# Kernel optimization log

Measured on AMD Instinct MI355X. Metric: run time of the kernel, lower is better.

Reference implementation:

```python
import jax, jax.numpy as jnp
import numpy as np

SEQ, BATCH, EMBED = 1024, 2, 768
E = 16            # num_experts = m * N = 2 * 8
FFN_H = 1536      # expert_dim = ceil(3072 / 2)
K_SHARED = 1
K_ROUTE = 3       # (m * top_k) - k_shared = 4 - 1
LN_EPS = 1e-5
NEG_INF = -1e9


def setup_inputs() -> dict:
    key = jax.random.key(0)
    ks = jax.random.split(key, 4)
    x = jax.random.normal(ks[0], (SEQ, BATCH, EMBED), dtype=jnp.float32)
    gate_w = jax.random.normal(ks[1], (EMBED, E), dtype=jnp.float32) * 0.02
    gate_b = jnp.zeros((E,), jnp.float32)
    fc1_w = jax.random.normal(ks[2], (E, EMBED, FFN_H), dtype=jnp.float32) * 0.02
    fc1_b = jnp.zeros((E, FFN_H), jnp.float32)
    ln_w = jnp.ones((E, FFN_H), jnp.float32)
    ln_b = jnp.zeros((E, FFN_H), jnp.float32)
    fc2_w = jax.random.normal(ks[3], (E, FFN_H, EMBED), dtype=jnp.float32) * 0.02
    fc2_b = jnp.zeros((E, EMBED), jnp.float32)
    return {"x": x, "gate_w": gate_w, "gate_b": gate_b,
            "fc1_w": fc1_w, "fc1_b": fc1_b, "ln_w": ln_w, "ln_b": ln_b,
            "fc2_w": fc2_w, "fc2_b": fc2_b}


def reference(x, gate_w, gate_b, fc1_w, fc1_b, ln_w, ln_b, fc2_w, fc2_b):
    S, B, D = x.shape
    T = S * B
    xf = x.reshape(T, D)

    # --- gating: mask shared-expert logits, softmax, top-k over routed probs ---
    scores = xf @ gate_w + gate_b                      # [T, E]
    scores = scores.at[:, :K_SHARED].set(NEG_INF)
    probs = jax.nn.softmax(scores, axis=-1)
    topv, topi = jax.lax.top_k(probs, K_ROUTE)         # [T, K_ROUTE]

    # combine weights: gate prob for selected routed experts, 1.0 for shared experts
    combine = jnp.zeros((T, E), xf.dtype)
    combine = combine.at[jnp.arange(T)[:, None], topi].add(topv)
    combine = combine.at[:, :K_SHARED].add(1.0)        # shared expert(s), weight 1

    # --- per-expert FFN (dense over experts; combine zeros out unselected) ---
    h = jnp.einsum('td,edh->eth', xf, fc1_w) + fc1_b[:, None, :]   # [E, T, H]
    h = jax.nn.gelu(h, approximate=False)              # torch nn.GELU = exact erf
    mu = h.mean(-1, keepdims=True)
    var = h.var(-1, keepdims=True)
    h = (h - mu) * jax.lax.rsqrt(var + LN_EPS) * ln_w[:, None, :] + ln_b[:, None, :]
    y = jnp.einsum('eth,ehd->etd', h, fc2_w) + fc2_b[:, None, :]   # [E, T, D]

    # --- scatter-add combine (gate-weighted sum over experts) ---
    out = jnp.einsum('te,etd->td', combine, y)
    return out.reshape(S, B, D)
```

## Files before the change

kernel.cpp:

```cpp
#include <hip/hip_runtime.h>
#include <cmath>

#define T_TOK 2048
#define D_EMB 768
#define H_FFN 1536
#define NE    16
#define NPAIR (T_TOK * 4)

typedef __attribute__((ext_vector_type(8))) short          short8;
typedef __attribute__((ext_vector_type(8))) unsigned short ushort8;
typedef __attribute__((ext_vector_type(4))) unsigned short ushort4v;
typedef __attribute__((ext_vector_type(4))) float          floatx4;

__device__ __forceinline__ float bf2f(unsigned short u) {
  union { unsigned int i; float f; } v; v.i = ((unsigned int)u) << 16; return v.f;
}
__device__ __forceinline__ unsigned short f2bf(float f) {
  union { float f; unsigned int i; } v; v.f = f;
  unsigned int r = v.i + 0x7fffu + ((v.i >> 16) & 1u);
  return (unsigned short)(r >> 16);
}

__global__ __launch_bounds__(64) void sniff_kernel(
    const unsigned int* __restrict__ x, int* __restrict__ flag)
{
  int lane = threadIdx.x;
  int c = 0;
  for (int i = 0; i < 8; i++) {
    unsigned int w = x[i * 64 + lane];
    unsigned int e = (w >> 7) & 0xFFu;
    c += (e >= 100u && e <= 140u) ? 1 : 0;
  }
  for (int off = 32; off > 0; off >>= 1) c += __shfl_down(c, off);
  if (lane == 0) *flag = (c > 300) ? 1 : 0;
}

__global__ __launch_bounds__(256) void conv_kernel(
    const float* __restrict__ x, const float* __restrict__ fc1b,
    const float* __restrict__ lnw, const float* __restrict__ lnb,
    const float* __restrict__ fc2b,
    unsigned short* __restrict__ dx, unsigned short* __restrict__ dfc1b,
    unsigned short* __restrict__ dlnw, unsigned short* __restrict__ dlnb,
    unsigned short* __restrict__ dfc2b, const int* __restrict__ flag)
{
  if (*flag) return;
  int g = blockIdx.x * 256 + threadIdx.x;
#pragma unroll
  for (int i = 0; i < 3; i++) dx[g + i * 524288] = f2bf(x[g + i * 524288]);
  if (g < 24576) { dfc1b[g] = f2bf(fc1b[g]); dlnw[g] = f2bf(lnw[g]); dlnb[g] = f2bf(lnb[g]); }
  if (g < 12288) dfc2b[g] = f2bf(fc2b[g]);
}

template<int R, int C>
__global__ __launch_bounds__(256) void transpose_kernel(
    const unsigned short* __restrict__ srcB, const float* __restrict__ srcF,
    const int* __restrict__ flag, unsigned short* __restrict__ dst)
{
  __shared__ __align__(16) unsigned short tile[64][72];
  constexpr int RT = R / 64, CT = C / 64;
  int bx  = blockIdx.x;
  int e   = bx / (RT * CT);
  int rem = bx % (RT * CT);
  int rt  = rem / CT, ct = rem % CT;
  int tid = threadIdx.x;
  int r   = tid >> 2;
  int c   = (tid & 3) * 16;
  int xr  = (r & 7) * 8;
  size_t sbase = ((size_t)e * R + rt * 64 + r) * C + ct * 64 + c;
  if (*flag) {
    ushort8 v0 = *(const ushort8*)(srcB + sbase);
    ushort8 v1 = *(const ushort8*)(srcB + sbase + 8);
    *(ushort8*)&tile[r][(c) ^ xr]     = v0;
    *(ushort8*)&tile[r][(c + 8) ^ xr] = v1;
  } else {
    unsigned short tmp[16];
#pragma unroll
    for (int q = 0; q < 4; q++) {
      floatx4 f = *(const floatx4*)(srcF + sbase + q * 4);
#pragma unroll
      for (int j = 0; j < 4; j++) tmp[q * 4 + j] = f2bf(f[j]);
    }
    *(ushort8*)&tile[r][(c) ^ xr]     = *(ushort8*)&tmp[0];
    *(ushort8*)&tile[r][(c + 8) ^ xr] = *(ushort8*)&tmp[8];
  }
  __syncthreads();
  int n  = tid >> 2;
  int k  = (tid & 3) * 16;
  unsigned short outv[16];
#pragma unroll
  for (int j = 0; j < 16; j++) {
    int kr = k + j;
    outv[j] = tile[kr][n ^ ((kr & 7) * 8)];
  }
  size_t dbase = ((size_t)e * C + ct * 64 + n) * R + rt * 64 + k;
  *(ushort8*)(dst + dbase)     = *(ushort8*)&outv[0];
  *(ushort8*)(dst + dbase + 8) = *(ushort8*)&outv[8];
}

__global__ __launch_bounds__(64) void gate_kernel(
    const unsigned short* __restrict__ x16, const float* __restrict__ x32,
    const unsigned short* __restrict__ gw16, const float* __restrict__ gw32,
    const unsigned short* __restrict__ gb16, const float* __restrict__ gb32,
    const int* __restrict__ flag,
    int* __restrict__ psel, float* __restrict__ pw)
{
  int t = blockIdx.x;
  int lane = threadIdx.x;
  int isbf = *flag;
  float acc[NE];
#pragma unroll
  for (int e = 0; e < NE; e++) acc[e] = 0.f;
  if (isbf) {
#pragma unroll
    for (int i = 0; i < D_EMB / 64; i++) {
      int d = i * 64 + lane;
      float xv = bf2f(x16[(size_t)t * D_EMB + d]);
      ushort8 g0 = *(const ushort8*)(gw16 + d * NE);
      ushort8 g1 = *(const ushort8*)(gw16 + d * NE + 8);
#pragma unroll
      for (int e = 0; e < 8; e++) acc[e]     += xv * bf2f(g0[e]);
#pragma unroll
      for (int e = 0; e < 8; e++) acc[8 + e] += xv * bf2f(g1[e]);
    }
  } else {
#pragma unroll
    for (int i = 0; i < D_EMB / 64; i++) {
      int d = i * 64 + lane;
      float xv = x32[(size_t)t * D_EMB + d];
#pragma unroll
      for (int q = 0; q < 4; q++) {
        floatx4 g = *(const floatx4*)(gw32 + d * NE + q * 4);
#pragma unroll
        for (int j = 0; j < 4; j++) acc[q * 4 + j] += xv * g[j];
      }
    }
  }
  __shared__ __align__(16) float sacc[64][NE + 1];
#pragma unroll
  for (int e = 0; e < NE; e++) sacc[lane][e] = acc[e];
  __syncthreads();
  int e = lane & 15, q = lane >> 4;
  float s = 0.f;
#pragma unroll
  for (int i = 0; i < 16; i++) s += sacc[q * 16 + i][e];
  s += __shfl_xor(s, 16);
  s += __shfl_xor(s, 32);
  float sv = s + (isbf ? bf2f(gb16[e]) : gb32[e]);
  if (e == 0) sv = -1e9f;
  float m = sv;
#pragma unroll
  for (int off = 8; off > 0; off >>= 1) m = fmaxf(m, __shfl_xor(m, off));
  float pe = expf(sv - m);
  float den = pe;
#pragma unroll
  for (int off = 8; off > 0; off >>= 1) den += __shfl_xor(den, off);
  float pr = pe / den;
  float val = (e == 0) ? -1.f : pr;
  int sel0, sel1, sel2; float sw0, sw1, sw2;
#pragma unroll
  for (int k = 0; k < 3; k++) {
    float bv = val; int bi = e;
#pragma unroll
    for (int off = 8; off > 0; off >>= 1) {
      float ov = __shfl_xor(bv, off);
      int   oi = __shfl_xor(bi, off);
      if (ov > bv || (ov == bv && oi < bi)) { bv = ov; bi = oi; }
    }
    if (k == 0) { sel0 = bi; sw0 = bv; }
    else if (k == 1) { sel1 = bi; sw1 = bv; }
    else { sel2 = bi; sw2 = bv; }
    if (e == bi) val = -1.f;
  }
  if (lane == 0) {
    psel[t * 4] = 0;    pw[t * 4] = 1.0f;
    psel[t * 4 + 1] = sel0; pw[t * 4 + 1] = sw0;
    psel[t * 4 + 2] = sel1; pw[t * 4 + 2] = sw1;
    psel[t * 4 + 3] = sel2; pw[t * 4 + 3] = sw2;
  }
}

__global__ __launch_bounds__(256) void bucket_kernel(
    const int* __restrict__ psel, int* __restrict__ cnt, int* __restrict__ plist)
{
  int e = blockIdx.x;
  int tid = threadIdx.x;
  int wave = tid >> 6, lane = tid & 63;
  __shared__ int wsum[4];
  __shared__ int base;
  if (tid == 0) base = 0;
  __syncthreads();
  for (int c0 = 0; c0 < NPAIR; c0 += 256) {
    bool mt = (psel[c0 + tid] == e);
    unsigned long long mask = __ballot(mt);
    int wcount = __popcll(mask);
    if (lane == 0) wsum[wave] = wcount;
    __syncthreads();
    int wpre = 0;
#pragma unroll
    for (int w = 0; w < 4; w++) if (w < wave) wpre += wsum[w];
    int total = wsum[0] + wsum[1] + wsum[2] + wsum[3];
    if (mt) {
      int off = __popcll(mask & ((1ULL << lane) - 1ULL));
      plist[e * T_TOK + base + wpre + off] = c0 + tid;
    }
    __syncthreads();
    if (tid == 0) base += total;
    __syncthreads();
  }
  if (tid == 0) cnt[e] = base;
}

template<int KDIM, int NDIM, bool GELU, bool HASBIAS, bool AROWDIV4, bool OUTF32>
__global__ __launch_bounds__(256) void moe_gemm(
    const unsigned short* __restrict__ AO, const unsigned short* __restrict__ AC,
    const unsigned short* __restrict__ BT,
    const unsigned short* __restrict__ biasO, const unsigned short* __restrict__ biasC,
    const int* __restrict__ flag,
    const int* __restrict__ cnt, const int* __restrict__ plist,
    unsigned short* __restrict__ outB, float* __restrict__ outF)
{
  const int NSP = NDIM / 128;
  int bx  = blockIdx.x;
  int e   = bx / (32 * NSP);
  int rem = bx % (32 * NSP);
  int mt  = rem / NSP;
  int ns  = rem % NSP;
  int count = cnt[e];
  if (mt * 64 >= count) return;
  const unsigned short* Abase   = (*flag) ? AO : AC;
  const unsigned short* biasAll = (*flag) ? biasO : biasC;

  __shared__ __align__(16) unsigned short sA[64][72];
  __shared__ __align__(16) unsigned short sB[128][72];
  __shared__ int sp[64];

  int tid = threadIdx.x;
  if (tid < 64) {
    int rg  = mt * 64 + tid;
    int idx = rg < count ? rg : count - 1;
    sp[tid] = plist[e * T_TOK + idx];
  }
  __syncthreads();

  int arow = tid >> 3;
  int ac8  = (tid & 7) * 8;
  int pr0 = sp[arow], pr1 = sp[arow + 32];
  const unsigned short* Aptr0 = Abase + (size_t)(AROWDIV4 ? (pr0 >> 2) : pr0) * KDIM + ac8;
  const unsigned short* Aptr1 = Abase + (size_t)(AROWDIV4 ? (pr1 >> 2) : pr1) * KDIM + ac8;
  int n0 = ns * 128;
  const unsigned short* Bptr =
      BT + ((size_t)e * NDIM + n0 + arow) * KDIM + ac8;

  int lane = tid & 63;
  int wave = tid >> 6;
  int wm   = (wave >> 1) * 32;
  int wn   = (wave & 1) * 64;
  int m16  = lane & 15;
  int quad = lane >> 4;

  floatx4 acc[2][4];
#pragma unroll
  for (int i = 0; i < 2; i++)
#pragma unroll
    for (int j = 0; j < 4; j++) acc[i][j] = (floatx4){0.f, 0.f, 0.f, 0.f};

  ushort8 pa0 = *(const ushort8*)(Aptr0);
  ushort8 pa1 = *(const ushort8*)(Aptr1);
  ushort8 pb0 = *(const ushort8*)(Bptr);
  ushort8 pb1 = *(const ushort8*)(Bptr + (size_t)32 * KDIM);
  ushort8 pb2 = *(const ushort8*)(Bptr + (size_t)64 * KDIM);
  ushort8 pb3 = *(const ushort8*)(Bptr + (size_t)96 * KDIM);

  for (int k0 = 0; k0 < KDIM; k0 += 64) {
    __syncthreads();
    *(ushort8*)&sA[arow][ac8]       = pa0;
    *(ushort8*)&sA[arow + 32][ac8]  = pa1;
    *(ushort8*)&sB[arow][ac8]       = pb0;
    *(ushort8*)&sB[arow + 32][ac8]  = pb1;
    *(ushort8*)&sB[arow + 64][ac8]  = pb2;
    *(ushort8*)&sB[arow + 96][ac8]  = pb3;
    __syncthreads();
    if (k0 + 64 < KDIM) {
      pa0 = *(const ushort8*)(Aptr0 + k0 + 64);
      pa1 = *(const ushort8*)(Aptr1 + k0 + 64);
      pb0 = *(const ushort8*)(Bptr + k0 + 64);
      pb1 = *(const ushort8*)(Bptr + k0 + 64 + (size_t)32 * KDIM);
      pb2 = *(const ushort8*)(Bptr + k0 + 64 + (size_t)64 * KDIM);
      pb3 = *(const ushort8*)(Bptr + k0 + 64 + (size_t)96 * KDIM);
    }
#pragma unroll
    for (int ks = 0; ks < 2; ks++) {
      short8 af0 = *(const short8*)&sA[wm + m16][ks * 32 + quad * 8];
      short8 af1 = *(const short8*)&sA[wm + 16 + m16][ks * 32 + quad * 8];
#pragma unroll
      for (int nt = 0; nt < 4; nt++) {
        short8 bfg = *(const short8*)&sB[wn + nt * 16 + m16][ks * 32 + quad * 8];
        acc[0][nt] = __builtin_amdgcn_mfma_f32_16x16x32_bf16(af0, bfg, acc[0][nt], 0, 0, 0);
        acc[1][nt] = __builtin_amdgcn_mfma_f32_16x16x32_bf16(af1, bfg, acc[1][nt], 0, 0, 0);
      }
    }
  }
#pragma unroll
  for (int sub = 0; sub < 2; sub++) {
#pragma unroll
    for (int nt = 0; nt < 4; nt++) {
#pragma unroll
      for (int r = 0; r < 4; r++) {
        int row_local = wm + sub * 16 + quad * 4 + r;
        int rg = mt * 64 + row_local;
        if (rg < count) {
          int col = n0 + wn + nt * 16 + m16;
          float v = acc[sub][nt][r];
          if (HASBIAS) v += bf2f(biasAll[e * NDIM + col]);
          if (GELU)    v = 0.5f * v * (1.f + erff(v * 0.70710678118654752f));
          int p = sp[row_local];
          if (OUTF32) outF[(size_t)p * NDIM + col] = v;
          else        outB[(size_t)p * NDIM + col] = f2bf(v);
        }
      }
    }
  }
}

__global__ __launch_bounds__(256) void ln_kernel(
    unsigned short* __restrict__ Hbuf,
    const unsigned short* __restrict__ lnwO, const unsigned short* __restrict__ lnwC,
    const unsigned short* __restrict__ lnbO, const unsigned short* __restrict__ lnbC,
    const int* __restrict__ psel, const float* __restrict__ pw,
    const int* __restrict__ flag)
{
  int p = blockIdx.x;
  int tid = threadIdx.x;
  int e = psel[p];
  int isbf = *flag;
  const unsigned short* lnw = isbf ? lnwO : lnwC;
  const unsigned short* lnb = isbf ? lnbO : lnbC;
  unsigned short* hr = Hbuf + (size_t)p * H_FFN;
  bool act = tid < 192;
  float v[8];
  float s = 0.f, sq = 0.f;
  if (act) {
    ushort8 hv = *(const ushort8*)(hr + tid * 8);
#pragma unroll
    for (int j = 0; j < 8; j++) { v[j] = bf2f(hv[j]); s += v[j]; sq += v[j] * v[j]; }
  }
#pragma unroll
  for (int off = 32; off > 0; off >>= 1) {
    s  += __shfl_down(s, off);
    sq += __shfl_down(sq, off);
  }
  __shared__ float red[8];
  int wave = tid >> 6, lane = tid & 63;
  if (lane == 0) { red[wave * 2] = s; red[wave * 2 + 1] = sq; }
  __syncthreads();
  __shared__ float mv[2];
  if (tid == 0) {
    float S = 0.f, Q = 0.f;
    for (int w = 0; w < 4; w++) { S += red[w * 2]; Q += red[w * 2 + 1]; }
    float mu  = S * (1.f / H_FFN);
    float var = Q * (1.f / H_FFN) - mu * mu;
    mv[0] = mu; mv[1] = rsqrtf(var + 1e-5f);
  }
  __syncthreads();
  if (act) {
    float mu = mv[0], rstd = mv[1];
    float w = pw[p];
    ushort8 lw = *(const ushort8*)(lnw + e * H_FFN + tid * 8);
    ushort8 lb = *(const ushort8*)(lnb + e * H_FFN + tid * 8);
    ushort8 o;
#pragma unroll
    for (int j = 0; j < 8; j++)
      o[j] = f2bf(((v[j] - mu) * rstd * bf2f(lw[j]) + bf2f(lb[j])) * w);
    *(ushort8*)(hr + tid * 8) = o;
  }
}

__global__ __launch_bounds__(256) void combine_kernel(
    const float* __restrict__ Y,
    const unsigned short* __restrict__ b2O, const unsigned short* __restrict__ b2C,
    const int* __restrict__ psel, const float* __restrict__ pw,
    unsigned short* __restrict__ out16, float* __restrict__ out32,
    const int* __restrict__ flag)
{
  int t = blockIdx.x;
  int tid = threadIdx.x;
  if (tid >= 192) return;
  int isbf = *flag;
  const unsigned short* b2 = isbf ? b2O : b2C;
  int e1 = psel[t * 4 + 1], e2 = psel[t * 4 + 2], e3 = psel[t * 4 + 3];
  float w1 = pw[t * 4 + 1], w2 = pw[t * 4 + 2], w3 = pw[t * 4 + 3];
  int d = tid * 4;
  const float* Yb = Y + (size_t)t * 4 * D_EMB + d;
  floatx4 y0 = *(const floatx4*)(Yb);
  floatx4 y1 = *(const floatx4*)(Yb + D_EMB);
  floatx4 y2 = *(const floatx4*)(Yb + 2 * D_EMB);
  floatx4 y3 = *(const floatx4*)(Yb + 3 * D_EMB);
  ushort4v b0 = *(const ushort4v*)(b2 + d);
  ushort4v bb1 = *(const ushort4v*)(b2 + e1 * D_EMB + d);
  ushort4v bb2 = *(const ushort4v*)(b2 + e2 * D_EMB + d);
  ushort4v bb3 = *(const ushort4v*)(b2 + e3 * D_EMB + d);
  if (isbf) {
    ushort4v o;
#pragma unroll
    for (int j = 0; j < 4; j++) {
      float a = y0[j] + y1[j] + y2[j] + y3[j] + bf2f(b0[j])
              + w1 * bf2f(bb1[j]) + w2 * bf2f(bb2[j]) + w3 * bf2f(bb3[j]);
      o[j] = f2bf(a);
    }
    *(ushort4v*)(out16 + (size_t)t * D_EMB + d) = o;
  } else {
    floatx4 o;
#pragma unroll
    for (int j = 0; j < 4; j++)
      o[j] = y0[j] + y1[j] + y2[j] + y3[j] + bf2f(b0[j])
           + w1 * bf2f(bb1[j]) + w2 * bf2f(bb2[j]) + w3 * bf2f(bb3[j]);
    *(floatx4*)(out32 + (size_t)t * D_EMB + d) = o;
  }
}

extern "C" void kernel_launch(void* const* d_in, const int* in_sizes, int n_in,
                              void* d_out, int out_size, void* d_ws, size_t ws_size,
                              hipStream_t stream)
{
  (void)in_sizes; (void)n_in; (void)out_size; (void)ws_size;
  char* ws = (char*)d_ws;
  int*   cnt   = (int*)ws;
  int*   plist = (int*)(ws + 256);
  int*   psel  = (int*)(ws + 131328);
  float* pw    = (float*)(ws + 164096);
  int*   flag  = (int*)(ws + 196864);
  unsigned short* fc1bC = (unsigned short*)(ws + 197120);
  unsigned short* lnwC  = (unsigned short*)(ws + 246272);
  unsigned short* lnbC  = (unsigned short*)(ws + 295424);
  unsigned short* fc2bC = (unsigned short*)(ws + 344576);
  unsigned short* xC    = (unsigned short*)(ws + 524288);
  unsigned short* Hbuf  = (unsigned short*)(ws + 3670016);
  float*          Ybuf  = (float*)(ws + 28835840);
  unsigned short* fc1T  = (unsigned short*)(ws + 54001664);
  unsigned short* fc2T  = (unsigned short*)(ws + 91750400);

  sniff_kernel<<<1, 64, 0, stream>>>((const unsigned int*)d_in[0], flag);

  conv_kernel<<<2048, 256, 0, stream>>>(
      (const float*)d_in[0], (const float*)d_in[4], (const float*)d_in[5],
      (const float*)d_in[6], (const float*)d_in[8],
      xC, fc1bC, lnwC, lnbC, fc2bC, flag);

  transpose_kernel<768, 1536><<<16 * 12 * 24, 256, 0, stream>>>(
      (const unsigned short*)d_in[3], (const float*)d_in[3], flag, fc1T);
  transpose_kernel<1536, 768><<<16 * 24 * 12, 256, 0, stream>>>(
      (const unsigned short*)d_in[7], (const float*)d_in[7], flag, fc2T);

  gate_kernel<<<T_TOK, 64, 0, stream>>>(
      (const unsigned short*)d_in[0], (const float*)d_in[0],
      (const unsigned short*)d_in[1], (const float*)d_in[1],
      (const unsigned short*)d_in[2], (const float*)d_in[2],
      flag, psel, pw);

  bucket_kernel<<<NE, 256, 0, stream>>>(psel, cnt, plist);

  moe_gemm<D_EMB, H_FFN, true, true, true, false>
      <<<NE * 32 * (H_FFN / 128), 256, 0, stream>>>(
      (const unsigned short*)d_in[0], xC, fc1T,
      (const unsigned short*)d_in[4], fc1bC,
      flag, cnt, plist, Hbuf, nullptr);

  ln_kernel<<<NPAIR, 256, 0, stream>>>(
      Hbuf,
      (const unsigned short*)d_in[5], lnwC,
      (const unsigned short*)d_in[6], lnbC,
      psel, pw, flag);

  moe_gemm<H_FFN, D_EMB, false, false, false, true>
      <<<NE * 32 * (D_EMB / 128), 256, 0, stream>>>(
      Hbuf, Hbuf, fc2T,
      nullptr, nullptr,
      flag, cnt, plist, nullptr, Ybuf);

  combine_kernel<<<T_TOK, 256, 0, stream>>>(
      Ybuf,
      (const unsigned short*)d_in[8], fc2bC,
      psel, pw,
      (unsigned short*)d_out, (float*)d_out, flag);
}
```

Baseline: 367.2 us.

## Enlarge MoE GEMM tile to 128x128 with direct global-to-LDS loads and XOR swizzle

```diff
diff --git a/kernel.cpp b/kernel.cpp
--- a/kernel.cpp
+++ b/kernel.cpp
@@ -19,6 +19,13 @@
   union { float f; unsigned int i; } v; v.f = f;
   unsigned int r = v.i + 0x7fffu + ((v.i >> 16) & 1u);
   return (unsigned short)(r >> 16);
+}
+
+__device__ __forceinline__ void gload16(const unsigned short* g, unsigned short* l) {
+  __builtin_amdgcn_global_load_lds(
+      (const __attribute__((address_space(1))) unsigned int*)g,
+      (__attribute__((address_space(3))) unsigned int*)l,
+      16, 0, 0);
 }
 
 __global__ __launch_bounds__(64) void sniff_kernel(
@@ -221,99 +228,98 @@
 {
   const int NSP = NDIM / 128;
   int bx  = blockIdx.x;
-  int e   = bx / (32 * NSP);
-  int rem = bx % (32 * NSP);
+  int e   = bx / (16 * NSP);
+  int rem = bx % (16 * NSP);
   int mt  = rem / NSP;
   int ns  = rem % NSP;
   int count = cnt[e];
-  if (mt * 64 >= count) return;
+  if (mt * 128 >= count) return;
   const unsigned short* Abase   = (*flag) ? AO : AC;
   const unsigned short* biasAll = (*flag) ? biasO : biasC;
 
-  __shared__ __align__(16) unsigned short sA[64][72];
-  __shared__ __align__(16) unsigned short sB[128][72];
-  __shared__ int sp[64];
+  __shared__ __align__(16) unsigned short sA[128 * 64];
+  __shared__ __align__(16) unsigned short sB[128 * 64];
+  __shared__ int sp[128];
 
   int tid = threadIdx.x;
-  if (tid < 64) {
-    int rg  = mt * 64 + tid;
+  if (tid < 128) {
+    int rg  = mt * 128 + tid;
     int idx = rg < count ? rg : count - 1;
     sp[tid] = plist[e * T_TOK + idx];
   }
   __syncthreads();
 
-  int arow = tid >> 3;
-  int ac8  = (tid & 7) * 8;
-  int pr0 = sp[arow], pr1 = sp[arow + 32];
-  const unsigned short* Aptr0 = Abase + (size_t)(AROWDIV4 ? (pr0 >> 2) : pr0) * KDIM + ac8;
-  const unsigned short* Aptr1 = Abase + (size_t)(AROWDIV4 ? (pr1 >> 2) : pr1) * KDIM + ac8;
-  int n0 = ns * 128;
-  const unsigned short* Bptr =
-      BT + ((size_t)e * NDIM + n0 + arow) * KDIM + ac8;
-
   int lane = tid & 63;
   int wave = tid >> 6;
-  int wm   = (wave >> 1) * 32;
-  int wn   = (wave & 1) * 64;
+  int n0   = ns * 128;
+
+  int lrow  = lane >> 3;
+  int lsch  = (lane & 7) ^ lrow;
+  const unsigned short* ag[4];
+  const unsigned short* bg[4];
+  unsigned short* la[4];
+  unsigned short* lb[4];
+#pragma unroll
+  for (int s = 0; s < 4; s++) {
+    int r  = wave * 32 + s * 8;
+    int p  = sp[r + lrow];
+    ag[s] = Abase + (size_t)(AROWDIV4 ? (p >> 2) : p) * KDIM + lsch * 8;
+    bg[s] = BT + ((size_t)e * NDIM + n0 + r + lrow) * KDIM + lsch * 8;
+    la[s] = sA + r * 64;
+    lb[s] = sB + r * 64;
+  }
+
   int m16  = lane & 15;
   int quad = lane >> 4;
-
-  floatx4 acc[2][4];
-#pragma unroll
-  for (int i = 0; i < 2; i++)
+  int wm   = (wave >> 1) * 64;
+  int wn   = (wave & 1) * 64;
+  int rsw  = (m16 & 7);
+
+  floatx4 acc[4][4];
+#pragma unroll
+  for (int i = 0; i < 4; i++)
 #pragma unroll
     for (int j = 0; j < 4; j++) acc[i][j] = (floatx4){0.f, 0.f, 0.f, 0.f};
 
-  ushort8 pa0 = *(const ushort8*)(Aptr0);
-  ushort8 pa1 = *(const ushort8*)(Aptr1);
-  ushort8 pb0 = *(const ushort8*)(Bptr);
-  ushort8 pb1 = *(const ushort8*)(Bptr + (size_t)32 * KDIM);
-  ushort8 pb2 = *(const ushort8*)(Bptr + (size_t)64 * KDIM);
-  ushort8 pb3 = *(const ushort8*)(Bptr + (size_t)96 * KDIM);
-
   for (int k0 = 0; k0 < KDIM; k0 += 64) {
+    if (k0) __syncthreads();
+#pragma unroll
+    for (int s = 0; s < 4; s++) gload16(ag[s] + k0, la[s]);
+#pragma unroll
+    for (int s = 0; s < 4; s++) gload16(bg[s] + k0, lb[s]);
     __syncthreads();
-    *(ushort8*)&sA[arow][ac8]       = pa0;
-    *(ushort8*)&sA[arow + 32][ac8]  = pa1;
-    *(ushort8*)&sB[arow][ac8]       = pb0;
-    *(ushort8*)&sB[arow + 32][ac8]  = pb1;
-    *(ushort8*)&sB[arow + 64][ac8]  = pb2;
-    *(ushort8*)&sB[arow + 96][ac8]  = pb3;
-    __syncthreads();
-    if (k0 + 64 < KDIM) {
-      pa0 = *(const ushort8*)(Aptr0 + k0 + 64);
-      pa1 = *(const ushort8*)(Aptr1 + k0 + 64);
-      pb0 = *(const ushort8*)(Bptr + k0 + 64);
-      pb1 = *(const ushort8*)(Bptr + k0 + 64 + (size_t)32 * KDIM);
-      pb2 = *(const ushort8*)(Bptr + k0 + 64 + (size_t)64 * KDIM);
-      pb3 = *(const ushort8*)(Bptr + k0 + 64 + (size_t)96 * KDIM);
-    }
 #pragma unroll
     for (int ks = 0; ks < 2; ks++) {
-      short8 af0 = *(const short8*)&sA[wm + m16][ks * 32 + quad * 8];
-      short8 af1 = *(const short8*)&sA[wm + 16 + m16][ks * 32 + quad * 8];
-#pragma unroll
-      for (int nt = 0; nt < 4; nt++) {
-        short8 bfg = *(const short8*)&sB[wn + nt * 16 + m16][ks * 32 + quad * 8];
-        acc[0][nt] = __builtin_amdgcn_mfma_f32_16x16x32_bf16(af0, bfg, acc[0][nt], 0, 0, 0);
-        acc[1][nt] = __builtin_amdgcn_mfma_f32_16x16x32_bf16(af1, bfg, acc[1][nt], 0, 0, 0);
-      }
-    }
-  }
-#pragma unroll
-  for (int sub = 0; sub < 2; sub++) {
-#pragma unroll
-    for (int nt = 0; nt < 4; nt++) {
-#pragma unroll
-      for (int r = 0; r < 4; r++) {
-        int row_local = wm + sub * 16 + quad * 4 + r;
-        int rg = mt * 64 + row_local;
-        if (rg < count) {
-          int col = n0 + wn + nt * 16 + m16;
-          float v = acc[sub][nt][r];
+      int ch = ((ks * 4 + quad) ^ rsw) * 8;
+      short8 af[4], bf[4];
+#pragma unroll
+      for (int m = 0; m < 4; m++)
+        af[m] = *(const short8*)(sA + (wm + m * 16 + m16) * 64 + ch);
+#pragma unroll
+      for (int n = 0; n < 4; n++)
+        bf[n] = *(const short8*)(sB + (wn + n * 16 + m16) * 64 + ch);
+#pragma unroll
+      for (int m = 0; m < 4; m++)
+#pragma unroll
+        for (int n = 0; n < 4; n++)
+          acc[m][n] = __builtin_amdgcn_mfma_f32_16x16x32_bf16(af[m], bf[n], acc[m][n], 0, 0, 0);
+    }
+  }
+
+#pragma unroll
+  for (int m = 0; m < 4; m++) {
+#pragma unroll
+    for (int r = 0; r < 4; r++) {
+      int row_local = wm + m * 16 + quad * 4 + r;
+      int rg = mt * 128 + row_local;
+      if (rg < count) {
+        int p = sp[row_local];
+#pragma unroll
+        for (int n = 0; n < 4; n++) {
+          int col = n0 + wn + n * 16 + m16;
+          float v = acc[m][n][r];
           if (HASBIAS) v += bf2f(biasAll[e * NDIM + col]);
           if (GELU)    v = 0.5f * v * (1.f + erff(v * 0.70710678118654752f));
-          int p = sp[row_local];
           if (OUTF32) outF[(size_t)p * NDIM + col] = v;
           else        outB[(size_t)p * NDIM + col] = f2bf(v);
         }
@@ -460,7 +466,7 @@
   bucket_kernel<<<NE, 256, 0, stream>>>(psel, cnt, plist);
 
   moe_gemm<D_EMB, H_FFN, true, true, true, false>
-      <<<NE * 32 * (H_FFN / 128), 256, 0, stream>>>(
+      <<<NE * 16 * (H_FFN / 128), 256, 0, stream>>>(
       (const unsigned short*)d_in[0], xC, fc1T,
       (const unsigned short*)d_in[4], fc1bC,
       flag, cnt, plist, Hbuf, nullptr);
@@ -472,7 +478,7 @@
       psel, pw, flag);
 
   moe_gemm<H_FFN, D_EMB, false, false, false, true>
-      <<<NE * 32 * (D_EMB / 128), 256, 0, stream>>>(
+      <<<NE * 16 * (D_EMB / 128), 256, 0, stream>>>(
       Hbuf, Hbuf, fc2T,
       nullptr, nullptr,
       flag, cnt, plist, nullptr, Ybuf);
```

Result: faster. 356.6 us (-2.9%).
